# Optimization experiments

Hardware: AMD Instinct MI355X
Metric: run time of the kernel (lower is better)

## Reference

```python
import jax, jax.numpy as jnp
import numpy as np

B, S, D, H = 4, 2048, 512, 8
DH = D // H  # 64


def setup_inputs() -> dict:
    key = jax.random.key(0)
    ks = jax.random.split(key, 7)
    scale = 1.0 / np.sqrt(D)
    return {
        "in_query": jax.random.normal(ks[0], (B, S, D), dtype=jnp.float32),
        "in_key": jax.random.normal(ks[1], (B, S, D), dtype=jnp.float32),
        "in_value": jax.random.normal(ks[2], (B, S, D), dtype=jnp.float32),
        "W_q": jax.random.normal(ks[3], (D, D), dtype=jnp.float32) * scale,
        "W_k": jax.random.normal(ks[4], (D, D), dtype=jnp.float32) * scale,
        "W_v": jax.random.normal(ks[5], (D, D), dtype=jnp.float32) * scale,
        "W_out": jax.random.normal(ks[6], (D, D), dtype=jnp.float32) * scale,
    }


def _split_heads(x):
    # [B, S, D] -> [B, H, S, DH]
    return x.reshape(B, S, H, DH).transpose(0, 2, 1, 3)


def reference(in_query, in_key, in_value, W_q, W_k, W_v, W_out):
    q = _split_heads(in_query @ W_q)   # [B,H,S,DH]
    k = _split_heads(in_key @ W_k)
    v = _split_heads(in_value @ W_v)
    scores = jnp.einsum("bhqd,bhkd->bhqk", q, k) / jnp.sqrt(jnp.float32(DH))
    attn = jax.nn.softmax(scores, axis=-1)  # dropout p=0 -> identity
    out = jnp.einsum("bhqk,bhkd->bhqd", attn, v)  # [B,H,S,DH]
    out = out.transpose(0, 2, 1, 3).reshape(B, S, D)
    return out @ W_out
```

## Files before the change

### kernel.cpp

```cpp
#include <hip/hip_runtime.h>
#include <hip/hip_bf16.h>
#include <cstdint>
#include <cstddef>


typedef __bf16 bf16;
typedef __attribute__((ext_vector_type(8))) __bf16 bf16x8;
typedef __attribute__((ext_vector_type(4))) __bf16 bf16x4;
typedef __attribute__((ext_vector_type(4))) float floatx4;

#define MFMA16(a, b, c) __builtin_amdgcn_mfma_f32_16x16x32_bf16(a, b, c, 0, 0, 0)

#define GLD16(gp, lp)                                              \
  __builtin_amdgcn_global_load_lds(                                \
      (const __attribute__((address_space(1))) unsigned int*)(gp), \
      (__attribute__((address_space(3))) unsigned int*)(lp), 16, 0, 0)

__device__ __forceinline__ void split2(float x, bf16& hi, bf16& lo) {
  hi = (bf16)x;
  lo = (bf16)(x - (float)hi);
}

__global__ __launch_bounds__(256) void k_split_w(
    const float* __restrict__ Wq, const float* __restrict__ Wk,
    const float* __restrict__ Wv, const float* __restrict__ Wo,
    bf16* __restrict__ wt_hi, bf16* __restrict__ wt_lo) {
  __shared__ float tile[64][65];
  const int w = blockIdx.z;
  const float* W = (w == 0) ? Wq : (w == 1) ? Wk : (w == 2) ? Wv : Wo;
  const int kb = blockIdx.y * 64, nb = blockIdx.x * 64;
  const int tid = threadIdx.x;
  const int col = tid & 63, rbase = tid >> 6;
#pragma unroll
  for (int i = 0; i < 16; i++) {
    int row = rbase + i * 4;
    tile[row][col] = W[(size_t)(kb + row) * 512 + nb + col];
  }
  __syncthreads();
#pragma unroll
  for (int i = 0; i < 16; i++) {
    int nrow = rbase + i * 4;
    float v = tile[col][nrow];
    bf16 hi, lo;
    split2(v, hi, lo);
    size_t o = (size_t)w * 262144 + (size_t)(nb + nrow) * 512 + (kb + col);
    wt_hi[o] = hi;
    wt_lo[o] = lo;
  }
}

__global__ __launch_bounds__(256, 2) void k_proj_qkv(
    const float* __restrict__ Xq, const float* __restrict__ Xk,
    const float* __restrict__ Xv,
    const bf16* __restrict__ wt_hi, const bf16* __restrict__ wt_lo,
    bf16* __restrict__ Q_hi, bf16* __restrict__ Q_lo,
    bf16* __restrict__ K, bf16* __restrict__ Vt) {
  const int P = blockIdx.x;
  const int c_all = P >> 5, within = P & 31;
  const int n_idx = within >> 3, i8 = within & 7;
  const int which = c_all >> 3;
  const int g = ((c_all & 7) << 3) | i8;
  const int m0 = g * 128, n0 = n_idx * 128;

  const float* X = (which == 0) ? Xq : (which == 1) ? Xk : Xv;
  const uint8_t* Bhb = (const uint8_t*)(wt_hi + (size_t)which * 262144);
  const uint8_t* Blb = (const uint8_t*)(wt_lo + (size_t)which * 262144);
  const uint8_t* Xb = (const uint8_t*)X;
  const int tid = threadIdx.x, wave = tid >> 6, lane = tid & 63;
  const int l15 = lane & 15, l4 = lane >> 4;
  const int Am0 = (wave & 1) * 64, Bn0 = (wave >> 1) * 64;

  __shared__ float sA[2][128 * 32];
  __shared__ bf16 sBh[2][128 * 32], sBl[2][128 * 32];

  int aoff[4], adst[4];
#pragma unroll
  for (int p = 0; p < 4; p++) {
    int slot = p * 256 + tid;
    int row = slot >> 3, phys = slot & 7, lg = phys ^ (row & 7);
    aoff[p] = (m0 + row) * 2048 + lg * 16;
    adst[p] = slot * 16;
  }
  int boff[2], bdst[2];
#pragma unroll
  for (int p = 0; p < 2; p++) {
    int slot = p * 256 + tid;
    int row = slot >> 2, phys = slot & 3, lg = phys ^ (row & 3);
    boff[p] = (n0 + row) * 1024 + lg * 16;
    bdst[p] = slot * 16;
  }

  floatx4 acc[4][4];
#pragma unroll
  for (int i = 0; i < 4; i++)
#pragma unroll
    for (int j = 0; j < 4; j++) acc[i][j] = {0.f, 0.f, 0.f, 0.f};

#pragma unroll
  for (int p = 0; p < 4; p++) GLD16(Xb + aoff[p], (char*)sA[0] + adst[p]);
#pragma unroll
  for (int p = 0; p < 2; p++) {
    GLD16(Bhb + boff[p], (char*)sBh[0] + bdst[p]);
    GLD16(Blb + boff[p], (char*)sBl[0] + bdst[p]);
  }
  __syncthreads();

  int cur = 0;
  for (int kb = 0; kb < 512; kb += 32) {
    if (kb + 32 < 512) {
      const int nx = cur ^ 1, nkb = kb + 32;
#pragma unroll
      for (int p = 0; p < 4; p++)
        GLD16(Xb + aoff[p] + nkb * 4, (char*)sA[nx] + adst[p]);
#pragma unroll
      for (int p = 0; p < 2; p++) {
        GLD16(Bhb + boff[p] + nkb * 2, (char*)sBh[nx] + bdst[p]);
        GLD16(Blb + boff[p] + nkb * 2, (char*)sBl[nx] + bdst[p]);
      }
    }
    const char* cA = (const char*)sA[cur];
    const char* cBh = (const char*)sBh[cur];
    const char* cBl = (const char*)sBl[cur];

    bf16x8 ah[4], al[4];
#pragma unroll
    for (int mt = 0; mt < 4; mt++) {
      int row = Am0 + mt * 16 + l15, r7 = row & 7;
      const float* f0 = (const float*)(cA + row * 128 + (((2 * l4) ^ r7) * 16));
      const float* f1 = (const float*)(cA + row * 128 + (((2 * l4 + 1) ^ r7) * 16));
#pragma unroll
      for (int j = 0; j < 4; j++) {
        bf16 h, l;
        split2(f0[j], h, l);
        ah[mt][j] = h; al[mt][j] = l;
        split2(f1[j], h, l);
        ah[mt][4 + j] = h; al[mt][4 + j] = l;
      }
    }
#pragma unroll
    for (int nt = 0; nt < 4; nt++) {
      int row = Bn0 + nt * 16 + l15, r3 = row & 3;
      bf16x8 bh = *(const bf16x8*)(cBh + row * 64 + ((l4 ^ r3) * 16));
      bf16x8 bl = *(const bf16x8*)(cBl + row * 64 + ((l4 ^ r3) * 16));
#pragma unroll
      for (int mt = 0; mt < 4; mt++) {
        acc[mt][nt] = MFMA16(ah[mt], bh, acc[mt][nt]);
        acc[mt][nt] = MFMA16(ah[mt], bl, acc[mt][nt]);
        acc[mt][nt] = MFMA16(al[mt], bh, acc[mt][nt]);
      }
    }
    __syncthreads();
    cur ^= 1;
  }

  const float scale = (which == 0) ? 0.125f : (which == 1) ? 1.44269504f : 1.0f;
#pragma unroll
  for (int mt = 0; mt < 4; mt++) {
#pragma unroll
    for (int nt = 0; nt < 4; nt++) {
      int m_base = m0 + Am0 + mt * 16 + l4 * 4;
      int n = n0 + Bn0 + nt * 16 + l15;
      int h = (n >> 6) & 7, d = n & 63;
      if (which == 2) {
        int kbase = m_base & 2047, b = m_base >> 11;
        int a32 = kbase & ~31, v = (kbase >> 2) & 7;
        int sbase = a32 + 8 * (v & 3) + 4 * (v >> 2);
        bf16x4 pv;
#pragma unroll
        for (int r = 0; r < 4; r++) pv[r] = (bf16)acc[mt][nt][r];
        *(bf16x4*)&Vt[((size_t)(b * 8 + h) * 64 + d) * 2048 + sbase] = pv;
      } else {
#pragma unroll
        for (int r = 0; r < 4; r++) {
          int m = m_base + r;
          int b = m >> 11, s = m & 2047;
          float v = acc[mt][nt][r] * scale;
          size_t o = ((size_t)(b * 8 + h) * 2048 + s) * 64 + d;
          if (which == 0) {
            bf16 hi, lo;
            split2(v, hi, lo);
            Q_hi[o] = hi; Q_lo[o] = lo;
          } else {
            K[o] = (bf16)v;
          }
        }
      }
    }
  }
}

__global__ __launch_bounds__(256, 2) void k_flash(
    const bf16* __restrict__ Q_hi, const bf16* __restrict__ Q_lo,
    const bf16* __restrict__ K, const bf16* __restrict__ Vt,
    bf16* __restrict__ O_hi, bf16* __restrict__ O_lo) {
  const int P = blockIdx.x;
  const int hi4 = P >> 8, rem = P & 255;
  const int qt = rem >> 3;
  const int bh = hi4 * 8 + (rem & 7);
  const int b = bh >> 3, h = bh & 7;
  const int tid = threadIdx.x, wave = tid >> 6, lane = tid & 63;
  const int l15 = lane & 15, l4 = lane >> 4;
  const int q0 = qt * 64;

  __shared__ char smem[2 * 32768 + 1024];
  float* lbuf = (float*)(smem + 65536);

  const uint8_t* Kb = (const uint8_t*)K + (size_t)bh * 2048 * 128;
  const uint8_t* Vb = (const uint8_t*)Vt + (size_t)bh * 64 * 4096;
  int koff[4], voff[4], dst[4];
#pragma unroll
  for (int p = 0; p < 4; p++) {
    int slot = p * 256 + tid;
    {
      int row = slot >> 3, phys = slot & 7, lg = phys ^ (row & 7);
      koff[p] = row * 128 + lg * 16;
    }
    {
      int row = slot >> 4, phys = slot & 15, lg = phys ^ (row & 15);
      voff[p] = row * 4096 + lg * 16;
    }
    dst[p] = slot * 16;
  }

#pragma unroll
  for (int p = 0; p < 4; p++) {
    GLD16(Kb + koff[p], smem + dst[p]);
    GLD16(Vb + voff[p], smem + 16384 + dst[p]);
  }

  bf16x8 qh[4][2], ql[4][2];
#pragma unroll
  for (int nt = 0; nt < 4; nt++) {
    const bf16* ph = Q_hi + ((size_t)bh * 2048 + q0 + nt * 16 + l15) * 64 + l4 * 8;
    const bf16* pl = Q_lo + ((size_t)bh * 2048 + q0 + nt * 16 + l15) * 64 + l4 * 8;
    qh[nt][0] = *(const bf16x8*)ph;
    qh[nt][1] = *(const bf16x8*)(ph + 32);
    ql[nt][0] = *(const bf16x8*)pl;
    ql[nt][1] = *(const bf16x8*)(pl + 32);
  }

  float lp[4] = {0.f, 0.f, 0.f, 0.f};
  floatx4 oacc[4][4];
#pragma unroll
  for (int i = 0; i < 4; i++)
#pragma unroll
    for (int j = 0; j < 4; j++) oacc[i][j] = {0.f, 0.f, 0.f, 0.f};

  __syncthreads();

  int cur = 0;
  for (int j0 = 0; j0 < 2048; j0 += 128) {
    if (j0 + 128 < 2048) {
      char* nb = smem + (cur ^ 1) * 32768;
      const size_t nj = (size_t)(j0 + 128);
#pragma unroll
      for (int p = 0; p < 4; p++) {
        GLD16(Kb + nj * 128 + koff[p], nb + dst[p]);
        GLD16(Vb + nj * 2 + voff[p], nb + 16384 + dst[p]);
      }
    }
    const char* sK = smem + cur * 32768;
    const char* sV = sK + 16384;

    floatx4 sc[2][4];
#pragma unroll
    for (int kt = 0; kt < 2; kt++)
#pragma unroll
      for (int nt = 0; nt < 4; nt++)
        sc[kt][nt] = {-24.f, -24.f, -24.f, -24.f};
#pragma unroll
    for (int kt = 0; kt < 2; kt++) {
      int row = wave * 32 + kt * 16 + l15;
      int r7 = row & 7;
#pragma unroll
      for (int ks = 0; ks < 2; ks++) {
        bf16x8 kh = *(const bf16x8*)(sK + (row * 128 + (((ks * 4 + l4) ^ r7) * 16)));
#pragma unroll
        for (int nt = 0; nt < 4; nt++) {
          sc[kt][nt] = MFMA16(kh, qh[nt][ks], sc[kt][nt]);
          sc[kt][nt] = MFMA16(kh, ql[nt][ks], sc[kt][nt]);
        }
      }
    }

    bf16x8 pf[4];
#pragma unroll
    for (int nt = 0; nt < 4; nt++) {
#pragma unroll
      for (int r = 0; r < 4; r++) {
        float p0 = __builtin_amdgcn_exp2f(sc[0][nt][r]);
        float p1 = __builtin_amdgcn_exp2f(sc[1][nt][r]);
        lp[nt] += p0 + p1;
        pf[nt][r] = (bf16)p0;
        pf[nt][4 + r] = (bf16)p1;
      }
    }

#pragma unroll
    for (int nt = 0; nt < 4; nt++) {
      int row = nt * 16 + l15;
      bf16x8 bv = *(const bf16x8*)(sV + (row * 256 + (((wave * 4 + l4) ^ l15) * 16)));
#pragma unroll
      for (int mq = 0; mq < 4; mq++)
        oacc[mq][nt] = MFMA16(pf[mq], bv, oacc[mq][nt]);
    }

    __syncthreads();
    cur ^= 1;
  }

#pragma unroll
  for (int nt = 0; nt < 4; nt++) {
    lp[nt] += __shfl_xor(lp[nt], 16, 64);
    lp[nt] += __shfl_xor(lp[nt], 32, 64);
  }
  if (l4 == 0) {
#pragma unroll
    for (int nt = 0; nt < 4; nt++) lbuf[wave * 64 + nt * 16 + l15] = lp[nt];
  }
  floatx4* red = (floatx4*)smem;
#pragma unroll
  for (int phase = 0; phase < 2; phase++) {
    if (wave >= 1) {
#pragma unroll
      for (int i = 0; i < 8; i++) {
        int mq = phase * 2 + (i >> 2);
        red[(wave - 1) * 512 + i * 64 + lane] = oacc[mq][i & 3];
      }
    }
    __syncthreads();
    if (wave == 0) {
#pragma unroll
      for (int i = 0; i < 8; i++) {
        int mq = phase * 2 + (i >> 2);
        oacc[mq][i & 3] += red[i * 64 + lane] + red[512 + i * 64 + lane] +
                           red[1024 + i * 64 + lane];
      }
    }
    __syncthreads();
  }
  if (wave == 0) {
    float lt[4];
#pragma unroll
    for (int nt = 0; nt < 4; nt++)
      lt[nt] = lbuf[nt * 16 + l15] + lbuf[64 + nt * 16 + l15] +
               lbuf[128 + nt * 16 + l15] + lbuf[192 + nt * 16 + l15];
    float rl[4][4];
#pragma unroll
    for (int mq = 0; mq < 4; mq++)
#pragma unroll
      for (int r = 0; r < 4; r++)
        rl[mq][r] = 1.0f / __shfl(lt[mq], (lane & 48) | (l4 * 4 + r), 64);
#pragma unroll
    for (int mq = 0; mq < 4; mq++) {
#pragma unroll
      for (int nt = 0; nt < 4; nt++) {
#pragma unroll
        for (int r = 0; r < 4; r++) {
          float v = oacc[mq][nt][r] * rl[mq][r];
          int gs = q0 + mq * 16 + l4 * 4 + r;
          int gd = h * 64 + nt * 16 + l15;
          size_t o = ((size_t)b * 2048 + gs) * 512 + gd;
          bf16 hi, lo;
          split2(v, hi, lo);
          O_hi[o] = hi;
          O_lo[o] = lo;
        }
      }
    }
  }
}

__global__ __launch_bounds__(256, 2) void k_proj_out(
    const bf16* __restrict__ O_hi, const bf16* __restrict__ O_lo,
    const bf16* __restrict__ wt_hi, const bf16* __restrict__ wt_lo,
    float* __restrict__ out) {
  const int P = blockIdx.x;
  const int c = P >> 5, within = P & 31;
  const int n_idx = within >> 3, i8 = within & 7;
  const int g = (c << 3) | i8;
  const int m0 = g * 128, n0 = n_idx * 128;

  const uint8_t* Ahb = (const uint8_t*)O_hi;
  const uint8_t* Alb = (const uint8_t*)O_lo;
  const uint8_t* Bhb = (const uint8_t*)(wt_hi + (size_t)3 * 262144);
  const uint8_t* Blb = (const uint8_t*)(wt_lo + (size_t)3 * 262144);
  const int tid = threadIdx.x, wave = tid >> 6, lane = tid & 63;
  const int l15 = lane & 15, l4 = lane >> 4;
  const int Am0 = (wave & 1) * 64, Bn0 = (wave >> 1) * 64;

  __shared__ bf16 sAh[2][128 * 32], sAl[2][128 * 32];
  __shared__ bf16 sBh[2][128 * 32], sBl[2][128 * 32];

  int aoff[2], boff[2], dst[2];
#pragma unroll
  for (int p = 0; p < 2; p++) {
    int slot = p * 256 + tid;
    int row = slot >> 2, phys = slot & 3, lg = phys ^ (row & 3);
    aoff[p] = (m0 + row) * 1024 + lg * 16;
    boff[p] = (n0 + row) * 1024 + lg * 16;
    dst[p] = slot * 16;
  }

  floatx4 acc[4][4];
#pragma unroll
  for (int i = 0; i < 4; i++)
#pragma unroll
    for (int j = 0; j < 4; j++) acc[i][j] = {0.f, 0.f, 0.f, 0.f};

#pragma unroll
  for (int p = 0; p < 2; p++) {
    GLD16(Ahb + aoff[p], (char*)sAh[0] + dst[p]);
    GLD16(Alb + aoff[p], (char*)sAl[0] + dst[p]);
    GLD16(Bhb + boff[p], (char*)sBh[0] + dst[p]);
    GLD16(Blb + boff[p], (char*)sBl[0] + dst[p]);
  }
  __syncthreads();

  int cur = 0;
  for (int kb = 0; kb < 512; kb += 32) {
    if (kb + 32 < 512) {
      const int nx = cur ^ 1, nkb = kb + 32;
#pragma unroll
      for (int p = 0; p < 2; p++) {
        GLD16(Ahb + aoff[p] + nkb * 2, (char*)sAh[nx] + dst[p]);
        GLD16(Alb + aoff[p] + nkb * 2, (char*)sAl[nx] + dst[p]);
        GLD16(Bhb + boff[p] + nkb * 2, (char*)sBh[nx] + dst[p]);
        GLD16(Blb + boff[p] + nkb * 2, (char*)sBl[nx] + dst[p]);
      }
    }
    const char* cAh = (const char*)sAh[cur];
    const char* cAl = (const char*)sAl[cur];
    const char* cBh = (const char*)sBh[cur];
    const char* cBl = (const char*)sBl[cur];

    bf16x8 ah[4], al[4];
#pragma unroll
    for (int mt = 0; mt < 4; mt++) {
      int row = Am0 + mt * 16 + l15, r3 = row & 3;
      ah[mt] = *(const bf16x8*)(cAh + row * 64 + ((l4 ^ r3) * 16));
      al[mt] = *(const bf16x8*)(cAl + row * 64 + ((l4 ^ r3) * 16));
    }
#pragma unroll
    for (int nt = 0; nt < 4; nt++) {
      int row = Bn0 + nt * 16 + l15, r3 = row & 3;
      bf16x8 bh = *(const bf16x8*)(cBh + row * 64 + ((l4 ^ r3) * 16));
      bf16x8 bl = *(const bf16x8*)(cBl + row * 64 + ((l4 ^ r3) * 16));
#pragma unroll
      for (int mt = 0; mt < 4; mt++) {
        acc[mt][nt] = MFMA16(ah[mt], bh, acc[mt][nt]);
        acc[mt][nt] = MFMA16(ah[mt], bl, acc[mt][nt]);
        acc[mt][nt] = MFMA16(al[mt], bh, acc[mt][nt]);
      }
    }
    __syncthreads();
    cur ^= 1;
  }
#pragma unroll
  for (int mt = 0; mt < 4; mt++) {
#pragma unroll
    for (int nt = 0; nt < 4; nt++) {
#pragma unroll
      for (int r = 0; r < 4; r++) {
        int m = m0 + Am0 + mt * 16 + l4 * 4 + r;
        int n = n0 + Bn0 + nt * 16 + l15;
        out[(size_t)m * 512 + n] = acc[mt][nt][r];
      }
    }
  }
}

extern "C" void kernel_launch(void* const* d_in, const int* in_sizes, int n_in,
                              void* d_out, int out_size, void* d_ws, size_t ws_size,
                              hipStream_t stream) {
  (void)in_sizes; (void)n_in; (void)out_size; (void)ws_size;
  const float* Xq = (const float*)d_in[0];
  const float* Xk = (const float*)d_in[1];
  const float* Xv = (const float*)d_in[2];
  const float* Wq = (const float*)d_in[3];
  const float* Wk = (const float*)d_in[4];
  const float* Wv = (const float*)d_in[5];
  const float* Wo = (const float*)d_in[6];
  float* out = (float*)d_out;

  char* ws = (char*)d_ws;
  size_t off = 0;
  auto alloc = [&](size_t n) {
    void* p = ws + off;
    off += (n + 255) & ~(size_t)255;
    return p;
  };
  const size_t NW = 4 * 262144;
  const size_t NE = 4194304;
  bf16* wt_hi = (bf16*)alloc(NW * 2);
  bf16* wt_lo = (bf16*)alloc(NW * 2);
  bf16* Qh = (bf16*)alloc(NE * 2);
  bf16* Ql = (bf16*)alloc(NE * 2);
  bf16* Kk = (bf16*)alloc(NE * 2);
  bf16* Vt = (bf16*)alloc(NE * 2);
  bf16* Oh = (bf16*)alloc(NE * 2);
  bf16* Ol = (bf16*)alloc(NE * 2);

  k_split_w<<<dim3(8, 8, 4), dim3(256), 0, stream>>>(Wq, Wk, Wv, Wo, wt_hi, wt_lo);
  k_proj_qkv<<<dim3(768), dim3(256), 0, stream>>>(Xq, Xk, Xv, wt_hi, wt_lo,
                                                  Qh, Ql, Kk, Vt);
  k_flash<<<dim3(1024), dim3(256), 0, stream>>>(Qh, Ql, Kk, Vt, Oh, Ol);
  k_proj_out<<<dim3(256), dim3(256), 0, stream>>>(Oh, Ol, wt_hi, wt_lo, out);
}
```

Before: 222.2 us.

## Split fp32 activations to bf16 hi/lo once at staging time in QKV projection

In the QKV projection GEMM, the A tile is now loaded from global memory into registers, split into bf16 hi/lo once, and written to swizzled LDS buffers. Previously fp32 was staged in LDS and each wave re-split its fragments on every k-step. This removes redundant conversions, since each A element was split by both N-waves, and halves the A LDS read bytes. The cost is register-staged loads in place of the async global_load_lds path for A, plus extra LDS writes after the MFMA block, which raises register pressure.

```diff
diff --git a/kernel.cpp b/kernel.cpp
--- a/kernel.cpp
+++ b/kernel.cpp
@@ -70,16 +70,17 @@
   const int l15 = lane & 15, l4 = lane >> 4;
   const int Am0 = (wave & 1) * 64, Bn0 = (wave >> 1) * 64;
 
-  __shared__ float sA[2][128 * 32];
-  __shared__ bf16 sBh[2][128 * 32], sBl[2][128 * 32];
-
-  int aoff[4], adst[4];
+  __shared__ bf16 sAh[2][4096], sAl[2][4096];
+  __shared__ bf16 sBh[2][4096], sBl[2][4096];
+
+  int aoffg[4], adst[4];
 #pragma unroll
   for (int p = 0; p < 4; p++) {
     int slot = p * 256 + tid;
-    int row = slot >> 3, phys = slot & 7, lg = phys ^ (row & 7);
-    aoff[p] = (m0 + row) * 2048 + lg * 16;
-    adst[p] = slot * 16;
+    int row = slot >> 3, q8 = slot & 7;
+    aoffg[p] = (m0 + row) * 2048 + q8 * 16;
+    int s16 = (q8 >> 1) ^ ((row >> 1) & 3);
+    adst[p] = row * 64 + s16 * 16 + (q8 & 1) * 8;
   }
   int boff[2], bdst[2];
 #pragma unroll
@@ -96,46 +97,58 @@
 #pragma unroll
     for (int j = 0; j < 4; j++) acc[i][j] = {0.f, 0.f, 0.f, 0.f};
 
-#pragma unroll
-  for (int p = 0; p < 4; p++) GLD16(Xb + aoff[p], (char*)sA[0] + adst[p]);
-#pragma unroll
-  for (int p = 0; p < 2; p++) {
-    GLD16(Bhb + boff[p], (char*)sBh[0] + bdst[p]);
-    GLD16(Blb + boff[p], (char*)sBl[0] + bdst[p]);
+  {
+    floatx4 ar[4];
+#pragma unroll
+    for (int p = 0; p < 4; p++)
+      ar[p] = *(const floatx4*)(Xb + aoffg[p]);
+#pragma unroll
+    for (int p = 0; p < 2; p++) {
+      GLD16(Bhb + boff[p], (char*)sBh[0] + bdst[p]);
+      GLD16(Blb + boff[p], (char*)sBl[0] + bdst[p]);
+    }
+#pragma unroll
+    for (int p = 0; p < 4; p++) {
+      bf16x4 hv, lv;
+#pragma unroll
+      for (int j = 0; j < 4; j++) {
+        bf16 h, l;
+        split2(ar[p][j], h, l);
+        hv[j] = h; lv[j] = l;
+      }
+      *(bf16x4*)((char*)sAh[0] + adst[p]) = hv;
+      *(bf16x4*)((char*)sAl[0] + adst[p]) = lv;
+    }
   }
   __syncthreads();
 
   int cur = 0;
   for (int kb = 0; kb < 512; kb += 32) {
-    if (kb + 32 < 512) {
-      const int nx = cur ^ 1, nkb = kb + 32;
+    const int nx = cur ^ 1;
+    const bool hn = (kb + 32) < 512;
+    floatx4 ar[4];
+    if (hn) {
 #pragma unroll
       for (int p = 0; p < 4; p++)
-        GLD16(Xb + aoff[p] + nkb * 4, (char*)sA[nx] + adst[p]);
+        ar[p] = *(const floatx4*)(Xb + aoffg[p] + (kb + 32) * 4);
 #pragma unroll
       for (int p = 0; p < 2; p++) {
-        GLD16(Bhb + boff[p] + nkb * 2, (char*)sBh[nx] + bdst[p]);
-        GLD16(Blb + boff[p] + nkb * 2, (char*)sBl[nx] + bdst[p]);
-      }
-    }
-    const char* cA = (const char*)sA[cur];
+        GLD16(Bhb + boff[p] + (kb + 32) * 2, (char*)sBh[nx] + bdst[p]);
+        GLD16(Blb + boff[p] + (kb + 32) * 2, (char*)sBl[nx] + bdst[p]);
+      }
+    }
+    const char* cAh = (const char*)sAh[cur];
+    const char* cAl = (const char*)sAl[cur];
     const char* cBh = (const char*)sBh[cur];
     const char* cBl = (const char*)sBl[cur];
 
     bf16x8 ah[4], al[4];
 #pragma unroll
     for (int mt = 0; mt < 4; mt++) {
-      int row = Am0 + mt * 16 + l15, r7 = row & 7;
-      const float* f0 = (const float*)(cA + row * 128 + (((2 * l4) ^ r7) * 16));
-      const float* f1 = (const float*)(cA + row * 128 + (((2 * l4 + 1) ^ r7) * 16));
-#pragma unroll
-      for (int j = 0; j < 4; j++) {
-        bf16 h, l;
-        split2(f0[j], h, l);
-        ah[mt][j] = h; al[mt][j] = l;
-        split2(f1[j], h, l);
-        ah[mt][4 + j] = h; al[mt][4 + j] = l;
-      }
+      int row = Am0 + mt * 16 + l15;
+      int sw = (l4 ^ ((row >> 1) & 3)) * 16;
+      ah[mt] = *(const bf16x8*)(cAh + row * 64 + sw);
+      al[mt] = *(const bf16x8*)(cAl + row * 64 + sw);
     }
 #pragma unroll
     for (int nt = 0; nt < 4; nt++) {
@@ -147,6 +160,20 @@
         acc[mt][nt] = MFMA16(ah[mt], bh, acc[mt][nt]);
         acc[mt][nt] = MFMA16(ah[mt], bl, acc[mt][nt]);
         acc[mt][nt] = MFMA16(al[mt], bh, acc[mt][nt]);
+      }
+    }
+    if (hn) {
+#pragma unroll
+      for (int p = 0; p < 4; p++) {
+        bf16x4 hv, lv;
+#pragma unroll
+        for (int j = 0; j < 4; j++) {
+          bf16 h, l;
+          split2(ar[p][j], h, l);
+          hv[j] = h; lv[j] = l;
+        }
+        *(bf16x4*)((char*)sAh[nx] + adst[p]) = hv;
+        *(bf16x4*)((char*)sAl[nx] + adst[p]) = lv;
       }
     }
     __syncthreads();
```

Measured after the change: 232.3 us. 1.05x slower.

## Drop double buffering and stage Q in LDS to fit three blocks per CU

Applied to the files above, without the earlier changes.

Both the QKV projection and flash-attention kernels switch from double-buffered LDS tiles to single buffers with a sync before and after each load. The flash kernel also moves its Q hi/lo fragments out of registers into LDS and reloads them each iteration. Launch bounds rise from 2 to 3 blocks per CU, so the smaller LDS and register footprint is meant to raise occupancy. In exchange, the overlap of global loads with MFMA work inside a block is lost and extra LDS reads and barriers are added.

```diff
diff --git a/kernel.cpp b/kernel.cpp
--- a/kernel.cpp
+++ b/kernel.cpp
@@ -49,7 +49,7 @@
   }
 }
 
-__global__ __launch_bounds__(256, 2) void k_proj_qkv(
+__global__ __launch_bounds__(256, 3) void k_proj_qkv(
     const float* __restrict__ Xq, const float* __restrict__ Xk,
     const float* __restrict__ Xv,
     const bf16* __restrict__ wt_hi, const bf16* __restrict__ wt_lo,
@@ -70,8 +70,8 @@
   const int l15 = lane & 15, l4 = lane >> 4;
   const int Am0 = (wave & 1) * 64, Bn0 = (wave >> 1) * 64;
 
-  __shared__ float sA[2][128 * 32];
-  __shared__ bf16 sBh[2][128 * 32], sBl[2][128 * 32];
+  __shared__ float sA[128 * 32];
+  __shared__ bf16 sBh[128 * 32], sBl[128 * 32];
 
   int aoff[4], adst[4];
 #pragma unroll
@@ -96,38 +96,23 @@
 #pragma unroll
     for (int j = 0; j < 4; j++) acc[i][j] = {0.f, 0.f, 0.f, 0.f};
 
-#pragma unroll
-  for (int p = 0; p < 4; p++) GLD16(Xb + aoff[p], (char*)sA[0] + adst[p]);
-#pragma unroll
-  for (int p = 0; p < 2; p++) {
-    GLD16(Bhb + boff[p], (char*)sBh[0] + bdst[p]);
-    GLD16(Blb + boff[p], (char*)sBl[0] + bdst[p]);
-  }
-  __syncthreads();
-
-  int cur = 0;
   for (int kb = 0; kb < 512; kb += 32) {
-    if (kb + 32 < 512) {
-      const int nx = cur ^ 1, nkb = kb + 32;
-#pragma unroll
-      for (int p = 0; p < 4; p++)
-        GLD16(Xb + aoff[p] + nkb * 4, (char*)sA[nx] + adst[p]);
-#pragma unroll
-      for (int p = 0; p < 2; p++) {
-        GLD16(Bhb + boff[p] + nkb * 2, (char*)sBh[nx] + bdst[p]);
-        GLD16(Blb + boff[p] + nkb * 2, (char*)sBl[nx] + bdst[p]);
-      }
-    }
-    const char* cA = (const char*)sA[cur];
-    const char* cBh = (const char*)sBh[cur];
-    const char* cBl = (const char*)sBl[cur];
+    __syncthreads();
+#pragma unroll
+    for (int p = 0; p < 4; p++) GLD16(Xb + aoff[p] + kb * 4, (char*)sA + adst[p]);
+#pragma unroll
+    for (int p = 0; p < 2; p++) {
+      GLD16(Bhb + boff[p] + kb * 2, (char*)sBh + bdst[p]);
+      GLD16(Blb + boff[p] + kb * 2, (char*)sBl + bdst[p]);
+    }
+    __syncthreads();
 
     bf16x8 ah[4], al[4];
 #pragma unroll
     for (int mt = 0; mt < 4; mt++) {
       int row = Am0 + mt * 16 + l15, r7 = row & 7;
-      const float* f0 = (const float*)(cA + row * 128 + (((2 * l4) ^ r7) * 16));
-      const float* f1 = (const float*)(cA + row * 128 + (((2 * l4 + 1) ^ r7) * 16));
+      const float* f0 = (const float*)((const char*)sA + row * 128 + (((2 * l4) ^ r7) * 16));
+      const float* f1 = (const float*)((const char*)sA + row * 128 + (((2 * l4 + 1) ^ r7) * 16));
 #pragma unroll
       for (int j = 0; j < 4; j++) {
         bf16 h, l;
@@ -140,8 +125,8 @@
 #pragma unroll
     for (int nt = 0; nt < 4; nt++) {
       int row = Bn0 + nt * 16 + l15, r3 = row & 3;
-      bf16x8 bh = *(const bf16x8*)(cBh + row * 64 + ((l4 ^ r3) * 16));
-      bf16x8 bl = *(const bf16x8*)(cBl + row * 64 + ((l4 ^ r3) * 16));
+      bf16x8 bh = *(const bf16x8*)((const char*)sBh + row * 64 + ((l4 ^ r3) * 16));
+      bf16x8 bl = *(const bf16x8*)((const char*)sBl + row * 64 + ((l4 ^ r3) * 16));
 #pragma unroll
       for (int mt = 0; mt < 4; mt++) {
         acc[mt][nt] = MFMA16(ah[mt], bh, acc[mt][nt]);
@@ -149,8 +134,6 @@
         acc[mt][nt] = MFMA16(al[mt], bh, acc[mt][nt]);
       }
     }
-    __syncthreads();
-    cur ^= 1;
   }
 
   const float scale = (which == 0) ? 0.125f : (which == 1) ? 1.44269504f : 1.0f;
@@ -189,7 +172,7 @@
   }
 }
 
-__global__ __launch_bounds__(256, 2) void k_flash(
+__global__ __launch_bounds__(256, 3) void k_flash(
     const bf16* __restrict__ Q_hi, const bf16* __restrict__ Q_lo,
     const bf16* __restrict__ K, const bf16* __restrict__ Vt,
     bf16* __restrict__ O_hi, bf16* __restrict__ O_lo) {
@@ -202,8 +185,8 @@
   const int l15 = lane & 15, l4 = lane >> 4;
   const int q0 = qt * 64;
 
-  __shared__ char smem[2 * 32768 + 1024];
-  float* lbuf = (float*)(smem + 65536);
+  __shared__ char smem[50176];
+  float* lbuf = (float*)(smem + 49152);
 
   const uint8_t* Kb = (const uint8_t*)K + (size_t)bh * 2048 * 128;
   const uint8_t* Vb = (const uint8_t*)Vt + (size_t)bh * 64 * 4096;
@@ -228,15 +211,19 @@
     GLD16(Vb + voff[p], smem + 16384 + dst[p]);
   }
 
-  bf16x8 qh[4][2], ql[4][2];
 #pragma unroll
   for (int nt = 0; nt < 4; nt++) {
-    const bf16* ph = Q_hi + ((size_t)bh * 2048 + q0 + nt * 16 + l15) * 64 + l4 * 8;
-    const bf16* pl = Q_lo + ((size_t)bh * 2048 + q0 + nt * 16 + l15) * 64 + l4 * 8;
-    qh[nt][0] = *(const bf16x8*)ph;
-    qh[nt][1] = *(const bf16x8*)(ph + 32);
-    ql[nt][0] = *(const bf16x8*)pl;
-    ql[nt][1] = *(const bf16x8*)(pl + 32);
+#pragma unroll
+    for (int ks = 0; ks < 2; ks++) {
+      const bf16* ph =
+          Q_hi + ((size_t)bh * 2048 + q0 + nt * 16 + l15) * 64 + ks * 32 + l4 * 8;
+      const bf16* pl =
+          Q_lo + ((size_t)bh * 2048 + q0 + nt * 16 + l15) * 64 + ks * 32 + l4 * 8;
+      *(bf16x8*)(smem + 32768 + ((nt * 2 + ks) * 64 + lane) * 16) =
+          *(const bf16x8*)ph;
+      *(bf16x8*)(smem + 40960 + ((nt * 2 + ks) * 64 + lane) * 16) =
+          *(const bf16x8*)pl;
+    }
   }
 
   float lp[4] = {0.f, 0.f, 0.f, 0.f};
@@ -248,19 +235,16 @@
 
   __syncthreads();
 
-  int cur = 0;
   for (int j0 = 0; j0 < 2048; j0 += 128) {
-    if (j0 + 128 < 2048) {
-      char* nb = smem + (cur ^ 1) * 32768;
-      const size_t nj = (size_t)(j0 + 128);
+    if (j0) {
+      __syncthreads();
 #pragma unroll
       for (int p = 0; p < 4; p++) {
-        GLD16(Kb + nj * 128 + koff[p], nb + dst[p]);
-        GLD16(Vb + nj * 2 + voff[p], nb + 16384 + dst[p]);
-      }
-    }
-    const char* sK = smem + cur * 32768;
-    const char* sV = sK + 16384;
+        GLD16(Kb + (size_t)j0 * 128 + koff[p], smem + dst[p]);
+        GLD16(Vb + (size_t)j0 * 2 + voff[p], smem + 16384 + dst[p]);
+      }
+      __syncthreads();
+    }
 
     floatx4 sc[2][4];
 #pragma unroll
@@ -269,17 +253,24 @@
       for (int nt = 0; nt < 4; nt++)
         sc[kt][nt] = {-24.f, -24.f, -24.f, -24.f};
 #pragma unroll
-    for (int kt = 0; kt < 2; kt++) {
-      int row = wave * 32 + kt * 16 + l15;
-      int r7 = row & 7;
-#pragma unroll
-      for (int ks = 0; ks < 2; ks++) {
-        bf16x8 kh = *(const bf16x8*)(sK + (row * 128 + (((ks * 4 + l4) ^ r7) * 16)));
-#pragma unroll
-        for (int nt = 0; nt < 4; nt++) {
-          sc[kt][nt] = MFMA16(kh, qh[nt][ks], sc[kt][nt]);
-          sc[kt][nt] = MFMA16(kh, ql[nt][ks], sc[kt][nt]);
-        }
+    for (int ks = 0; ks < 2; ks++) {
+      bf16x8 kh0, kh1;
+      {
+        int row = wave * 32 + l15, r7 = row & 7;
+        kh0 = *(const bf16x8*)(smem + row * 128 + (((ks * 4 + l4) ^ r7) * 16));
+      }
+      {
+        int row = wave * 32 + 16 + l15, r7 = row & 7;
+        kh1 = *(const bf16x8*)(smem + row * 128 + (((ks * 4 + l4) ^ r7) * 16));
+      }
+#pragma unroll
+      for (int nt = 0; nt < 4; nt++) {
+        bf16x8 qhf = *(const bf16x8*)(smem + 32768 + ((nt * 2 + ks) * 64 + lane) * 16);
+        bf16x8 qlf = *(const bf16x8*)(smem + 40960 + ((nt * 2 + ks) * 64 + lane) * 16);
+        sc[0][nt] = MFMA16(kh0, qhf, sc[0][nt]);
+        sc[0][nt] = MFMA16(kh0, qlf, sc[0][nt]);
+        sc[1][nt] = MFMA16(kh1, qhf, sc[1][nt]);
+        sc[1][nt] = MFMA16(kh1, qlf, sc[1][nt]);
       }
     }
 
@@ -299,14 +290,12 @@
 #pragma unroll
     for (int nt = 0; nt < 4; nt++) {
       int row = nt * 16 + l15;
-      bf16x8 bv = *(const bf16x8*)(sV + (row * 256 + (((wave * 4 + l4) ^ l15) * 16)));
+      bf16x8 bv = *(const bf16x8*)(smem + 16384 + row * 256 +
+                                   (((wave * 4 + l4) ^ l15) * 16));
 #pragma unroll
       for (int mq = 0; mq < 4; mq++)
         oacc[mq][nt] = MFMA16(pf[mq], bv, oacc[mq][nt]);
     }
-
-    __syncthreads();
-    cur ^= 1;
   }
 
 #pragma unroll
@@ -314,6 +303,7 @@
     lp[nt] += __shfl_xor(lp[nt], 16, 64);
     lp[nt] += __shfl_xor(lp[nt], 32, 64);
   }
+  __syncthreads();
   if (l4 == 0) {
 #pragma unroll
     for (int nt = 0; nt < 4; nt++) lbuf[wave * 64 + nt * 16 + l15] = lp[nt];
```

New measurement: 220.8 us. No clear change (-0.6%).
